# Kernel optimization log

Hardware: AMD Instinct MI355X
Metric: run time of the kernel (lower is better)

Reference implementation:

```python
import jax, jax.numpy as jnp
import numpy as np

MRG = 0.1
ALPHA = 32.0
STAT_WEIGHT = 0.01
STAT_ADJUST_WEIGHT = 0.15
COS_EPS = 1e-8  # torch F.cosine_similarity eps


def l2_norm(x):
    # matches torch l2_norm: x / sqrt(sum(x^2, axis=1) + 1e-12)
    normp = jnp.sum(x * x, axis=1) + 1e-12
    return x / jnp.sqrt(normp)[:, None]


def setup_inputs() -> dict:
    key = jax.random.key(0)
    kx, kt, kp, kc = jax.random.split(key, 4)
    B, C, D = 512, 50000, 128
    X = jax.random.normal(kx, (B, D), dtype=jnp.float32)
    T = jax.random.randint(kt, (B,), 0, C, dtype=jnp.int32)
    proxies = jax.random.normal(kp, (C, D), dtype=jnp.float32)
    class_centers = jax.random.normal(kc, (C, D), dtype=jnp.float32)
    return {"X": X, "T": T, "proxies": proxies, "class_centers": class_centers}


def reference(X, T, proxies, class_centers):
    C = proxies.shape[0]
    Xn = l2_norm(X)                      # (B, D)
    Pn = l2_norm(proxies)                # (C, D)
    cos = Xn @ Pn.T                      # (B, C)

    # ---- vectorized per-class statistics (replaces the Python loop) ----
    counts = jax.ops.segment_sum(jnp.ones(T.shape[0], jnp.float32), T, num_segments=C)
    sums = jax.ops.segment_sum(Xn, T, num_segments=C)          # (C, D)
    sqs = jax.ops.segment_sum(Xn * Xn, T, num_segments=C)      # (C, D)
    safe = jnp.maximum(counts, 1.0)[:, None]
    mean = sums / safe
    var = jnp.clip(sqs / safe - mean * mean, 1e-6, 10.0)        # biased var, clamped
    var_weight = 1.0 / (1.0 + var.mean(axis=1))                 # (C,)

    # cosine_similarity(P_norm[i], class_centers[i]) with torch eps semantics
    pnorm = jnp.maximum(jnp.sqrt(jnp.sum(Pn * Pn, axis=1)), COS_EPS)
    cnorm = jnp.maximum(jnp.sqrt(jnp.sum(class_centers * class_centers, axis=1)), COS_EPS)
    center_sim = jnp.sum(Pn * class_centers, axis=1) / (pnorm * cnorm)  # (C,)

    has_samples = counts > 0
    adj = jnp.where(has_samples, center_sim * var_weight * STAT_ADJUST_WEIGHT, 0.0)
    combined = cos + adj[None, :]        # (B, C)

    # ---- proxy-anchor exp-sum terms ----
    onehot = (T[:, None] == jnp.arange(C, dtype=T.dtype)[None, :])  # (B, C) bool
    pos_exp = jnp.exp(-ALPHA * (combined - MRG))
    neg_exp = jnp.exp(ALPHA * (combined + MRG))
    P_sim_sum = jnp.sum(jnp.where(onehot, pos_exp, 0.0), axis=0)    # (C,)
    N_sim_sum = jnp.sum(jnp.where(onehot, 0.0, neg_exp), axis=0)    # (C,)

    num_valid = jnp.sum(has_samples).astype(jnp.float32)
    pos_term = jnp.sum(jnp.log1p(P_sim_sum)) / num_valid
    neg_term = jnp.sum(jnp.log1p(N_sim_sum)) / jnp.float32(C)

    center_reg = jnp.mean(jnp.abs(class_centers))
    return pos_term + neg_term + STAT_WEIGHT * center_reg
```

## Files before the change

### kernel.cpp

```cpp
#include <hip/hip_runtime.h>
#include <math.h>

#define ALPHA 32.0f
#define MRG 0.1f
#define STAT_WEIGHT 0.01f
#define STAT_ADJ_W 0.15f
#define COS_EPS 1e-8f

typedef __attribute__((ext_vector_type(8))) short bf16x8;
typedef __attribute__((ext_vector_type(4))) float f32x4;
typedef __attribute__((ext_vector_type(4))) unsigned int u32x4;

__device__ __forceinline__ ushort f2bf(float f) {
    unsigned u = __float_as_uint(f);
    return (ushort)((u + 0x7FFFu + ((u >> 16) & 1u)) >> 16);
}
__device__ __forceinline__ unsigned pk2(float a, float b) {
    return (unsigned)f2bf(a) | ((unsigned)f2bf(b) << 16);
}

__device__ __forceinline__ float bred128(float v, float* sm, int d) {
    #pragma unroll
    for (int off = 1; off < 64; off <<= 1) v += __shfl_xor(v, off);
    if ((d & 63) == 0) sm[d >> 6] = v;
    __syncthreads();
    float r = sm[0] + sm[1];
    __syncthreads();
    return r;
}

__global__ void k_stats(const float* __restrict__ X, const float* __restrict__ proxies,
                        const float* __restrict__ cc, const int* __restrict__ T,
                        ushort* __restrict__ Xn16, float* __restrict__ adj,
                        float* __restrict__ zbase, int nzero,
                        float* __restrict__ cabs_part, int C, int B) {
    const int b = blockIdx.x, d = threadIdx.x;
    __shared__ int Tl[512];
    __shared__ float sm[2];
    __shared__ float smc[2];
    __shared__ int mlist[512];
    __shared__ int mcnt;

    for (int i = b * 128 + d; i < nzero; i += B * 128) zbase[i] = 0.f;

    for (int i = d; i < B; i += 128) Tl[i] = T[i];
    if (d == 0) mcnt = 0;

    float cabs = 0.f;
    {
        const float4* cp = (const float4*)cc;
        const int n4 = C * 32;
        for (int i = b * 128 + d; i < n4; i += B * 128) {
            float4 v = cp[i];
            cabs += fabsf(v.x) + fabsf(v.y) + fabsf(v.z) + fabsf(v.w);
        }
    }
    #pragma unroll
    for (int off = 1; off < 64; off <<= 1) cabs += __shfl_xor(cabs, off);
    if ((d & 63) == 0) smc[d >> 6] = cabs;
    __syncthreads();
    if (d == 0) cabs_part[b] = smc[0] + smc[1];

    const int c = Tl[b];

    float x = X[(size_t)b * 128 + d];
    float n2 = bred128(x * x, sm, d);
    float xn = x * rsqrtf(n2 + 1e-12f);
    const int pk = ((((d >> 3) ^ (b & 15)) << 3) | (d & 7));
    Xn16[(size_t)b * 128 + pk] = f2bf(xn);

    for (int j = d; j < B; j += 128)
        if (Tl[j] == c) mlist[atomicAdd(&mcnt, 1)] = j;
    __syncthreads();
    const int cnt = mcnt;
    int minj = mlist[0];
    for (int i = 1; i < cnt; ++i) minj = min(minj, mlist[i]);
    if (minj != b) return;

    float sd = 0.f, qd = 0.f;
    int prev = -1;
    for (int rank = 0; rank < cnt; ++rank) {
        int cur = 0x7fffffff;
        for (int i = 0; i < cnt; ++i) { int v = mlist[i]; if (v > prev && v < cur) cur = v; }
        prev = cur;
        float xj = X[(size_t)cur * 128 + d];
        float nj = bred128(xj * xj, sm, d);
        float xnj = xj * rsqrtf(nj + 1e-12f);
        sd += xnj; qd += xnj * xnj;
    }
    float fc = (float)cnt;
    float m = sd / fc;
    float var = fminf(fmaxf(qd / fc - m * m, 1e-6f), 10.0f);
    float sv = bred128(var, sm, d);

    float p  = proxies[(size_t)c * 128 + d];
    float cv = cc[(size_t)c * 128 + d];
    float s2 = bred128(p * p, sm, d);
    float c2 = bred128(cv * cv, sm, d);
    float pc = bred128(p * cv, sm, d);
    if (d == 0) {
        float inv = rsqrtf(s2 + 1e-12f);
        float pn = fmaxf(sqrtf(s2) * inv, COS_EPS);
        float cn = fmaxf(sqrtf(c2), COS_EPS);
        float censim = (pc * inv) / (pn * cn);
        float vw = 1.0f / (1.0f + sv * (1.0f / 128.0f));
        adj[c] = censim * vw * STAT_ADJ_W;
    }
}

__launch_bounds__(256, 2)
__global__ void k_main(const float* __restrict__ proxies, const ushort* __restrict__ Xsw,
                       const int* __restrict__ T, float* __restrict__ PN,
                       int C) {
    const int tid = threadIdx.x, lane = tid & 63, wv = tid >> 6;
    const int nlo = lane & 15, quad = lane >> 4;
    const int c0 = blockIdx.x * 128;
    const int q = blockIdx.y;
    const int r0 = q * 128;

    __shared__ ushort Sx[16384];
    __shared__ alignas(16) int Tl[128];
    if (tid < 128) Tl[tid] = T[r0 + tid];

    float* P = PN + (size_t)(q >> 1) * 2 * C;
    float* N = P + C;

    const int cls0 = c0 + wv * 32 + nlo;
    const int cls1 = cls0 + 16;
    bf16x8 bfr[2][4];
    #pragma unroll
    for (int t = 0; t < 2; ++t) {
        int cls = c0 + wv * 32 + t * 16 + nlo;
        int cl = (cls < C) ? cls : C - 1;
        const float4* pr = (const float4*)(proxies + (size_t)cl * 128);
        float4 v0[4], v1[4];
        float s2 = 0.f;
        #pragma unroll
        for (int ks = 0; ks < 4; ++ks) {
            v0[ks] = pr[ks * 8 + quad * 2];
            v1[ks] = pr[ks * 8 + quad * 2 + 1];
            s2 += v0[ks].x*v0[ks].x + v0[ks].y*v0[ks].y + v0[ks].z*v0[ks].z + v0[ks].w*v0[ks].w
                + v1[ks].x*v1[ks].x + v1[ks].y*v1[ks].y + v1[ks].z*v1[ks].z + v1[ks].w*v1[ks].w;
        }
        s2 += __shfl_xor(s2, 16);
        s2 += __shfl_xor(s2, 32);
        float pin = rsqrtf(s2 + 1e-12f);
        #pragma unroll
        for (int ks = 0; ks < 4; ++ks) {
            u32x4 u;
            u.x = pk2(v0[ks].x * pin, v0[ks].y * pin);
            u.y = pk2(v0[ks].z * pin, v0[ks].w * pin);
            u.z = pk2(v1[ks].x * pin, v1[ks].y * pin);
            u.w = pk2(v1[ks].z * pin, v1[ks].w * pin);
            bfr[t][ks] = __builtin_bit_cast(bf16x8, u);
        }
    }

    int fro[4];
    #pragma unroll
    for (int ks = 0; ks < 4; ++ks)
        fro[ks] = nlo * 128 + (((ks * 4 + quad) ^ nlo) << 3);

    const uint4* gX = (const uint4*)Xsw + q * 2048;
    uint4 s0, s1, s2v, s3;
    #define LOADV(ch) { const uint4* p_ = gX + (ch) * 1024 + tid; \
                        s0 = p_[0]; s1 = p_[256]; s2v = p_[512]; s3 = p_[768]; }
    #define WRITEV(bi) { uint4* q_ = (uint4*)&Sx[(bi) * 8192]; \
                         q_[tid] = s0; q_[tid + 256] = s1; q_[tid + 512] = s2v; q_[tid + 768] = s3; }
    LOADV(0); WRITEV(0); LOADV(1);
    __syncthreads();

    float pp0 = 0.f, np0 = 0.f, pp1 = 0.f, np1 = 0.f;
    for (int chunk = 0; chunk < 2; ++chunk) {
        const int bo = chunk * 8192;
        if (chunk < 1) WRITEV(1);
        #pragma unroll
        for (int rt = 0; rt < 4; ++rt) {
            const ushort* sb = &Sx[bo + rt * 2048];
            bf16x8 a0 = *(const bf16x8*)&sb[fro[0]];
            bf16x8 a1 = *(const bf16x8*)&sb[fro[1]];
            bf16x8 a2 = *(const bf16x8*)&sb[fro[2]];
            bf16x8 a3 = *(const bf16x8*)&sb[fro[3]];
            f32x4 acc0 = {0.f,0.f,0.f,0.f}, acc1 = {0.f,0.f,0.f,0.f};
            acc0 = __builtin_amdgcn_mfma_f32_16x16x32_bf16(a0, bfr[0][0], acc0, 0, 0, 0);
            acc1 = __builtin_amdgcn_mfma_f32_16x16x32_bf16(a0, bfr[1][0], acc1, 0, 0, 0);
            acc0 = __builtin_amdgcn_mfma_f32_16x16x32_bf16(a1, bfr[0][1], acc0, 0, 0, 0);
            acc1 = __builtin_amdgcn_mfma_f32_16x16x32_bf16(a1, bfr[1][1], acc1, 0, 0, 0);
            acc0 = __builtin_amdgcn_mfma_f32_16x16x32_bf16(a2, bfr[0][2], acc0, 0, 0, 0);
            acc1 = __builtin_amdgcn_mfma_f32_16x16x32_bf16(a2, bfr[1][2], acc1, 0, 0, 0);
            acc0 = __builtin_amdgcn_mfma_f32_16x16x32_bf16(a3, bfr[0][3], acc0, 0, 0, 0);
            acc1 = __builtin_amdgcn_mfma_f32_16x16x32_bf16(a3, bfr[1][3], acc1, 0, 0, 0);

            int4 t4 = *(const int4*)&Tl[chunk * 64 + rt * 16 + quad * 4];
            int tvs[4] = {t4.x, t4.y, t4.z, t4.w};
            #pragma unroll
            for (int r = 0; r < 4; ++r) {
                { bool po = (tvs[r] == cls0); float v = acc0[r];
                  float e = __expf(po ? -ALPHA * (v - MRG) : ALPHA * (v + MRG));
                  pp0 += po ? e : 0.f; np0 += po ? 0.f : e; }
                { bool po = (tvs[r] == cls1); float v = acc1[r];
                  float e = __expf(po ? -ALPHA * (v - MRG) : ALPHA * (v + MRG));
                  pp1 += po ? e : 0.f; np1 += po ? 0.f : e; }
            }
        }
        __syncthreads();
    }
    #undef LOADV
    #undef WRITEV

    pp0 += __shfl_xor(pp0, 16); pp0 += __shfl_xor(pp0, 32);
    np0 += __shfl_xor(np0, 16); np0 += __shfl_xor(np0, 32);
    pp1 += __shfl_xor(pp1, 16); pp1 += __shfl_xor(pp1, 32);
    np1 += __shfl_xor(np1, 16); np1 += __shfl_xor(np1, 32);
    if (quad == 0) {
        if (cls0 < C) { atomicAdd(&P[cls0], pp0); atomicAdd(&N[cls0], np0); }
        if (cls1 < C) { atomicAdd(&P[cls1], pp1); atomicAdd(&N[cls1], np1); }
    }
}

__launch_bounds__(256)
__global__ void k_fin(const float* __restrict__ PN, const float* __restrict__ adj,
                      const float* __restrict__ cabs_part, float* __restrict__ scal,
                      float* __restrict__ out, int C, int nfin) {
    const int tid = threadIdx.x, lane = tid & 63, wv = tid >> 6;
    const int c = blockIdx.x * 256 + tid;
    __shared__ float red[4][3];
    float lp = 0.f, ln = 0.f, nv = 0.f;
    if (c < C) {
        float p = PN[c] + PN[2 * (size_t)C + c];
        float n = PN[(size_t)C + c] + PN[3 * (size_t)C + c];
        float a = 0.f;
        if (p > 0.f) { a = adj[c]; nv = 1.f; }
        lp = log1pf(p * __expf(-ALPHA * a));
        ln = log1pf(n * __expf( ALPHA * a));
    }
    #pragma unroll
    for (int off = 1; off < 64; off <<= 1) {
        lp += __shfl_xor(lp, off);
        ln += __shfl_xor(ln, off);
        nv += __shfl_xor(nv, off);
    }
    if (lane == 0) { red[wv][0] = lp; red[wv][1] = ln; red[wv][2] = nv; }
    __syncthreads();
    if (tid == 0) {
        atomicAdd(&scal[0], red[0][0] + red[1][0] + red[2][0] + red[3][0]);
        atomicAdd(&scal[1], red[0][1] + red[1][1] + red[2][1] + red[3][1]);
        atomicAdd(&scal[3], red[0][2] + red[1][2] + red[2][2] + red[3][2]);
    }
    if (blockIdx.x == 0) {
        float cb = cabs_part[tid] + cabs_part[tid + 256];
        #pragma unroll
        for (int off = 1; off < 64; off <<= 1) cb += __shfl_xor(cb, off);
        __syncthreads();
        if (lane == 0) red[wv][0] = cb;
        __syncthreads();
        if (tid == 0) atomicAdd(&scal[2], red[0][0] + red[1][0] + red[2][0] + red[3][0]);
    }
    if (tid == 0) {
        __threadfence();
        unsigned old = atomicAdd((unsigned*)(scal + 4), 1u);
        if (old == (unsigned)(nfin - 1)) {
            float S0 = atomicAdd(&scal[0], 0.f);
            float S1 = atomicAdd(&scal[1], 0.f);
            float S2 = atomicAdd(&scal[2], 0.f);
            float S3 = atomicAdd(&scal[3], 0.f);
            out[0] = S0 / S3 + S1 / (float)C + STAT_WEIGHT * (S2 / ((float)C * 128.f));
        }
    }
}

extern "C" void kernel_launch(void* const* d_in, const int* in_sizes, int n_in,
                              void* d_out, int out_size, void* d_ws, size_t ws_size,
                              hipStream_t stream) {
    const float* X       = (const float*)d_in[0];
    const int*   T       = (const int*)d_in[1];
    const float* proxies = (const float*)d_in[2];
    const float* cc      = (const float*)d_in[3];
    float* out = (float*)d_out;

    const int B = in_sizes[1];
    const int D = in_sizes[0] / B;
    const int C = in_sizes[2] / D;

    float*  PN   = (float*)d_ws;
    float*  scal = PN + 4 * (size_t)C;
    float*  cabs_part = scal + 8;
    float*  adj  = cabs_part + 512;
    ushort* Xn16 = (ushort*)(adj + C);

    const int nblk  = (C + 127) / 128;
    const int nfin  = (C + 255) / 256;
    const int nzero = 4 * C + 8;

    k_stats<<<B, 128, 0, stream>>>(X, proxies, cc, T, Xn16, adj, PN, nzero,
                                   cabs_part, C, B);
    k_main<<<dim3(nblk, 4), 256, 0, stream>>>(proxies, Xn16, T, PN, C);
    k_fin<<<nfin, 256, 0, stream>>>(PN, adj, cabs_part, scal, out, C, nfin);
}
```

Measured before the change: 131.8 us.

## Make k_main persistent with resident X half, direct stores instead of atomics

k_main becomes a persistent grid of 256x2 blocks. Each block loads one half of the bf16 X (256 rows, 64KB LDS) once, then loops over class slices. Each block now covers all 256 rows of its half, so partial P/N sums are written with plain stores and no atomics. This also removes the large zero-fill of the PN workspace in k_stats. The cost is more LDS per block, which lowers occupancy, and less parallelism across blocks, with 512 persistent blocks against about 782 slices and an uneven tail.

Result: no change. 130.6 us (-0.9%).

```diff
diff --git a/kernel.cpp b/kernel.cpp
--- a/kernel.cpp
+++ b/kernel.cpp
@@ -32,8 +32,8 @@
 __global__ void k_stats(const float* __restrict__ X, const float* __restrict__ proxies,
                         const float* __restrict__ cc, const int* __restrict__ T,
                         ushort* __restrict__ Xn16, float* __restrict__ adj,
-                        float* __restrict__ zbase, int nzero,
-                        float* __restrict__ cabs_part, int C, int B) {
+                        float* __restrict__ scal, float* __restrict__ cabs_part,
+                        int C, int B) {
     const int b = blockIdx.x, d = threadIdx.x;
     __shared__ int Tl[512];
     __shared__ float sm[2];
@@ -41,7 +41,7 @@
     __shared__ int mlist[512];
     __shared__ int mcnt;
 
-    for (int i = b * 128 + d; i < nzero; i += B * 128) zbase[i] = 0.f;
+    if (b == 0 && d < 8) scal[d] = 0.f;
 
     for (int i = d; i < B; i += 128) Tl[i] = T[i];
     if (d == 0) mcnt = 0;
@@ -111,72 +111,69 @@
 __launch_bounds__(256, 2)
 __global__ void k_main(const float* __restrict__ proxies, const ushort* __restrict__ Xsw,
                        const int* __restrict__ T, float* __restrict__ PN,
-                       int C) {
+                       int C, int nslice) {
     const int tid = threadIdx.x, lane = tid & 63, wv = tid >> 6;
     const int nlo = lane & 15, quad = lane >> 4;
-    const int c0 = blockIdx.x * 128;
-    const int q = blockIdx.y;
-    const int r0 = q * 128;
-
-    __shared__ ushort Sx[16384];
-    __shared__ alignas(16) int Tl[128];
-    if (tid < 128) Tl[tid] = T[r0 + tid];
-
-    float* P = PN + (size_t)(q >> 1) * 2 * C;
-    float* N = P + C;
-
-    const int cls0 = c0 + wv * 32 + nlo;
-    const int cls1 = cls0 + 16;
-    bf16x8 bfr[2][4];
-    #pragma unroll
-    for (int t = 0; t < 2; ++t) {
-        int cls = c0 + wv * 32 + t * 16 + nlo;
-        int cl = (cls < C) ? cls : C - 1;
-        const float4* pr = (const float4*)(proxies + (size_t)cl * 128);
-        float4 v0[4], v1[4];
-        float s2 = 0.f;
+    const int half = blockIdx.y;
+
+    __shared__ ushort Sx[32768];
+    __shared__ alignas(16) int Tl[256];
+
+    {
+        const uint4* src = (const uint4*)Xsw + half * 4096;
+        uint4* dst = (uint4*)Sx;
         #pragma unroll
-        for (int ks = 0; ks < 4; ++ks) {
-            v0[ks] = pr[ks * 8 + quad * 2];
-            v1[ks] = pr[ks * 8 + quad * 2 + 1];
-            s2 += v0[ks].x*v0[ks].x + v0[ks].y*v0[ks].y + v0[ks].z*v0[ks].z + v0[ks].w*v0[ks].w
-                + v1[ks].x*v1[ks].x + v1[ks].y*v1[ks].y + v1[ks].z*v1[ks].z + v1[ks].w*v1[ks].w;
-        }
-        s2 += __shfl_xor(s2, 16);
-        s2 += __shfl_xor(s2, 32);
-        float pin = rsqrtf(s2 + 1e-12f);
-        #pragma unroll
-        for (int ks = 0; ks < 4; ++ks) {
-            u32x4 u;
-            u.x = pk2(v0[ks].x * pin, v0[ks].y * pin);
-            u.y = pk2(v0[ks].z * pin, v0[ks].w * pin);
-            u.z = pk2(v1[ks].x * pin, v1[ks].y * pin);
-            u.w = pk2(v1[ks].z * pin, v1[ks].w * pin);
-            bfr[t][ks] = __builtin_bit_cast(bf16x8, u);
-        }
-    }
+        for (int k = 0; k < 16; ++k) dst[tid + k * 256] = src[tid + k * 256];
+    }
+    Tl[tid] = T[half * 256 + tid];
+    __syncthreads();
+
+    float* PA = PN + (size_t)half * 2 * C;
+    float* NA = PA + C;
 
     int fro[4];
     #pragma unroll
     for (int ks = 0; ks < 4; ++ks)
         fro[ks] = nlo * 128 + (((ks * 4 + quad) ^ nlo) << 3);
 
-    const uint4* gX = (const uint4*)Xsw + q * 2048;
-    uint4 s0, s1, s2v, s3;
-    #define LOADV(ch) { const uint4* p_ = gX + (ch) * 1024 + tid; \
-                        s0 = p_[0]; s1 = p_[256]; s2v = p_[512]; s3 = p_[768]; }
-    #define WRITEV(bi) { uint4* q_ = (uint4*)&Sx[(bi) * 8192]; \
-                         q_[tid] = s0; q_[tid + 256] = s1; q_[tid + 512] = s2v; q_[tid + 768] = s3; }
-    LOADV(0); WRITEV(0); LOADV(1);
-    __syncthreads();
-
-    float pp0 = 0.f, np0 = 0.f, pp1 = 0.f, np1 = 0.f;
-    for (int chunk = 0; chunk < 2; ++chunk) {
-        const int bo = chunk * 8192;
-        if (chunk < 1) WRITEV(1);
+    for (int s = blockIdx.x; s < nslice; s += gridDim.x) {
+        const int c0 = s * 128;
+        const int cls0 = c0 + wv * 32 + nlo;
+        const int cls1 = cls0 + 16;
+
+        bf16x8 bfr[2][4];
         #pragma unroll
-        for (int rt = 0; rt < 4; ++rt) {
-            const ushort* sb = &Sx[bo + rt * 2048];
+        for (int t = 0; t < 2; ++t) {
+            int cls = c0 + wv * 32 + t * 16 + nlo;
+            int cl = (cls < C) ? cls : C - 1;
+            const float4* pr = (const float4*)(proxies + (size_t)cl * 128);
+            float4 v0[4], v1[4];
+            float s2 = 0.f;
+            #pragma unroll
+            for (int ks = 0; ks < 4; ++ks) {
+                v0[ks] = pr[ks * 8 + quad * 2];
+                v1[ks] = pr[ks * 8 + quad * 2 + 1];
+                s2 += v0[ks].x*v0[ks].x + v0[ks].y*v0[ks].y + v0[ks].z*v0[ks].z + v0[ks].w*v0[ks].w
+                    + v1[ks].x*v1[ks].x + v1[ks].y*v1[ks].y + v1[ks].z*v1[ks].z + v1[ks].w*v1[ks].w;
+            }
+            s2 += __shfl_xor(s2, 16);
+            s2 += __shfl_xor(s2, 32);
+            float pin = rsqrtf(s2 + 1e-12f);
+            #pragma unroll
+            for (int ks = 0; ks < 4; ++ks) {
+                u32x4 u;
+                u.x = pk2(v0[ks].x * pin, v0[ks].y * pin);
+                u.y = pk2(v0[ks].z * pin, v0[ks].w * pin);
+                u.z = pk2(v1[ks].x * pin, v1[ks].y * pin);
+                u.w = pk2(v1[ks].z * pin, v1[ks].w * pin);
+                bfr[t][ks] = __builtin_bit_cast(bf16x8, u);
+            }
+        }
+
+        float pp0 = 0.f, np0 = 0.f, pp1 = 0.f, np1 = 0.f;
+        #pragma unroll 4
+        for (int rt = 0; rt < 16; ++rt) {
+            const ushort* sb = &Sx[rt * 2048];
             bf16x8 a0 = *(const bf16x8*)&sb[fro[0]];
             bf16x8 a1 = *(const bf16x8*)&sb[fro[1]];
             bf16x8 a2 = *(const bf16x8*)&sb[fro[2]];
@@ -191,7 +188,7 @@
             acc0 = __builtin_amdgcn_mfma_f32_16x16x32_bf16(a3, bfr[0][3], acc0, 0, 0, 0);
             acc1 = __builtin_amdgcn_mfma_f32_16x16x32_bf16(a3, bfr[1][3], acc1, 0, 0, 0);
 
-            int4 t4 = *(const int4*)&Tl[chunk * 64 + rt * 16 + quad * 4];
+            int4 t4 = *(const int4*)&Tl[rt * 16 + quad * 4];
             int tvs[4] = {t4.x, t4.y, t4.z, t4.w};
             #pragma unroll
             for (int r = 0; r < 4; ++r) {
@@ -203,18 +200,15 @@
                   pp1 += po ? e : 0.f; np1 += po ? 0.f : e; }
             }
         }
-        __syncthreads();
-    }
-    #undef LOADV
-    #undef WRITEV
-
-    pp0 += __shfl_xor(pp0, 16); pp0 += __shfl_xor(pp0, 32);
-    np0 += __shfl_xor(np0, 16); np0 += __shfl_xor(np0, 32);
-    pp1 += __shfl_xor(pp1, 16); pp1 += __shfl_xor(pp1, 32);
-    np1 += __shfl_xor(np1, 16); np1 += __shfl_xor(np1, 32);
-    if (quad == 0) {
-        if (cls0 < C) { atomicAdd(&P[cls0], pp0); atomicAdd(&N[cls0], np0); }
-        if (cls1 < C) { atomicAdd(&P[cls1], pp1); atomicAdd(&N[cls1], np1); }
+
+        pp0 += __shfl_xor(pp0, 16); pp0 += __shfl_xor(pp0, 32);
+        np0 += __shfl_xor(np0, 16); np0 += __shfl_xor(np0, 32);
+        pp1 += __shfl_xor(pp1, 16); pp1 += __shfl_xor(pp1, 32);
+        np1 += __shfl_xor(np1, 16); np1 += __shfl_xor(np1, 32);
+        if (quad == 0) {
+            if (cls0 < C) { PA[cls0] = pp0; NA[cls0] = np0; }
+            if (cls1 < C) { PA[cls1] = pp1; NA[cls1] = np1; }
+        }
     }
 }
 
@@ -288,12 +282,11 @@
     float*  adj  = cabs_part + 512;
     ushort* Xn16 = (ushort*)(adj + C);
 
-    const int nblk  = (C + 127) / 128;
-    const int nfin  = (C + 255) / 256;
-    const int nzero = 4 * C + 8;
-
-    k_stats<<<B, 128, 0, stream>>>(X, proxies, cc, T, Xn16, adj, PN, nzero,
+    const int nslice = (C + 127) / 128;
+    const int nfin   = (C + 255) / 256;
+
+    k_stats<<<B, 128, 0, stream>>>(X, proxies, cc, T, Xn16, adj, scal,
                                    cabs_part, C, B);
-    k_main<<<dim3(nblk, 4), 256, 0, stream>>>(proxies, Xn16, T, PN, C);
+    k_main<<<dim3(256, 2), 256, 0, stream>>>(proxies, Xn16, T, PN, C, nslice);
     k_fin<<<nfin, 256, 0, stream>>>(PN, adj, cabs_part, scal, out, C, nfin);
 }
```
